# Performance work log

Hardware: AMD Instinct MI355X
Metric: run time of the kernel (lower is better)

Reference implementation:

```python
import jax, jax.numpy as jnp
import numpy as np

N, F_NODE, F_EDGE = 1024, 64, 32
F_IN = 2 * F_NODE + F_EDGE  # 160


def setup_inputs() -> dict:
    key = jax.random.key(0)
    ks = jax.random.split(key, 6)
    H = jax.random.normal(ks[0], (N, F_NODE), dtype=jnp.float32)
    A = jax.random.randint(ks[1], (N, N), 0, 2).astype(jnp.float32)
    E = jax.random.normal(ks[2], (N, N, F_EDGE), dtype=jnp.float32)
    # params: reset_parameters_uniform -> U(-s, s), s = 1/sqrt(dim0)
    s = 1.0 / np.sqrt(F_IN)
    W = jax.random.uniform(ks[3], (F_IN, F_NODE), jnp.float32, -s, s)
    W_att = jax.random.uniform(ks[4], (F_IN, F_NODE), jnp.float32, -s, s)
    sb = 1.0 / np.sqrt(F_NODE)
    bias = jax.random.uniform(ks[5], (F_NODE,), jnp.float32, -sb, sb)
    return {"H": H, "A": A, "E": E, "W": W, "W_att": W_att, "bias": bias}


def reference(H, A, E, W, W_att, bias):
    n = H.shape[0]
    # all-pairs concat: HE[a,b] = [H[a], H[b], E[a,b]]  -> [N, N, 2F+Fe]
    H_row = jnp.broadcast_to(H[:, None, :], (n, n, H.shape[1]))  # H2: repeat over dim 1
    H_col = jnp.broadcast_to(H[None, :, :], (n, n, H.shape[1]))  # H1: repeat over dim 0
    HE = jnp.concatenate([H_row, H_col, E], axis=2) * A[:, :, None]
    Hp = jnp.einsum('abi,ij->abj', HE, W) + bias
    Ha = jnp.einsum('abi,ij->abj', HE, W_att) + bias
    gated = jax.nn.relu(Hp) * jax.nn.sigmoid(Ha)
    return jnp.sum(gated, axis=1)
```

## Files before the change

### kernel.cpp

```cpp
#include <hip/hip_runtime.h>

#define NN 1024
#define FN 64
#define FE 32
#define FIN 160
#define NS 2

typedef __bf16 bf16x8 __attribute__((ext_vector_type(8)));
typedef short  short8 __attribute__((ext_vector_type(8)));
typedef float  f32x4  __attribute__((ext_vector_type(4)));

static __device__ __forceinline__ unsigned short f2b(float x){
    unsigned int u = __float_as_uint(x);
    unsigned int r = (u + 0x7fffu + ((u >> 16) & 1u)) >> 16;
    return (unsigned short)r;
}

static __device__ __forceinline__ float fast_sigmoid(float y){
    return __builtin_amdgcn_rcpf(1.0f + __expf(-y));
}

static __device__ __forceinline__ bf16x8 ldfrag(const unsigned short* p){
    return __builtin_bit_cast(bf16x8, *(const short8*)(p));
}

static __device__ __forceinline__ unsigned packtrunc(float lo, float hi){
    return __builtin_amdgcn_perm(__float_as_uint(hi), __float_as_uint(lo), 0x07060302u);
}

__global__ void prep(const float* __restrict__ H, const float* __restrict__ W,
                     const float* __restrict__ Wa,
                     unsigned short* __restrict__ Hb,
                     unsigned short* __restrict__ WtE,
                     unsigned short* __restrict__ WtA){
    int bid = blockIdx.x, tid = threadIdx.x;
    if (bid < 64){
        int i = (bid*256 + tid)*4;
        float4 v = *(const float4*)(H + i);
        ushort4 o;
        o.x = f2b(v.x); o.y = f2b(v.y); o.z = f2b(v.z); o.w = f2b(v.w);
        *(ushort4*)(Hb + i) = o;
    } else {
        const float* src = (bid == 64) ? W : Wa;
        unsigned short* dst = (bid == 64) ? WtE : WtA;
        for (int idx = tid; idx < FIN*FN; idx += 256){
            int k = idx >> 6, j = idx & 63;
            dst[j*FIN + k] = f2b(src[idx]);
        }
    }
}

__global__ void compact(const float* __restrict__ A, unsigned short* __restrict__ idxg,
                        int* __restrict__ cnt){
    int a = blockIdx.x, tid = threadIdx.x;
    int wave = tid >> 6, lane = tid & 63;
    int b0 = wave*256 + lane*4;
    float4 v = *(const float4*)(A + (size_t)a*NN + b0);
    unsigned short loc[4]; int m = 0;
    if (v.x != 0.f) loc[m++] = (unsigned short)(b0);
    if (v.y != 0.f) loc[m++] = (unsigned short)(b0 + 1);
    if (v.z != 0.f) loc[m++] = (unsigned short)(b0 + 2);
    if (v.w != 0.f) loc[m++] = (unsigned short)(b0 + 3);
    int sc = m;
    #pragma unroll
    for (int d = 1; d < 64; d <<= 1){
        int t = __shfl_up(sc, d, 64);
        sc += (lane >= d) ? t : 0;
    }
    __shared__ int wsum[4];
    if (lane == 63) wsum[wave] = sc;
    __syncthreads();
    int base = 0;
    #pragma unroll
    for (int w = 0; w < 4; w++) base += (w < wave) ? wsum[w] : 0;
    int pos = base + sc - m;
    for (int i = 0; i < m; i++) idxg[(size_t)a*NN + pos + i] = loc[i];
    if (tid == 0) cnt[a] = wsum[0] + wsum[1] + wsum[2] + wsum[3];
}

__global__ __launch_bounds__(256, 3) void mga_main(
    const float* __restrict__ E,
    const unsigned short* __restrict__ Hb,
    const unsigned short* __restrict__ WtE, const unsigned short* __restrict__ WtA,
    const unsigned short* __restrict__ idxg, const int* __restrict__ cnt,
    const float* __restrict__ bias, float* __restrict__ part)
{
    int bid  = blockIdx.x;
    int a    = bid >> 1, s = bid & 1;
    int tid  = threadIdx.x;
    int wave = tid >> 6, lane = tid & 63;
    int col  = lane & 15, quad = lane >> 4;
    int half = wave >> 1, mh = wave & 1;

    __shared__ unsigned short lidx[512];
    __shared__ float red[16*FN];

    int c1   = cnt[a];
    int hlen = (c1 + 1) >> 1;
    int win  = s ? hlen : 0;
    int len  = s ? (c1 - hlen) : hlen;
    int npad = (len + 63) & ~63;

    for (int i = tid; i < npad; i += 256){
        int off = (i < len) ? i : (len - 1);
        lidx[i] = idxg[(size_t)a*NN + win + off];
    }

    bf16x8 Bw[2][3], Ba[2][3];
    #pragma unroll
    for (int tl = 0; tl < 2; tl++){
        int n = (2*half + tl)*16 + col;
        #pragma unroll
        for (int sg = 0; sg < 3; sg++){
            Bw[tl][sg] = ldfrag(WtE + n*FIN + (sg+2)*32 + quad*8);
            Ba[tl][sg] = ldfrag(WtA + n*FIN + (sg+2)*32 + quad*8);
        }
    }

    bf16x8 ha0 = ldfrag(Hb + a*FN + quad*8);
    bf16x8 ha1 = ldfrag(Hb + a*FN + 32 + quad*8);
    f32x4 cw[2], ca[2];
    float acc[2] = {0.f, 0.f};
    #pragma unroll
    for (int tl = 0; tl < 2; tl++){
        int n = (2*half + tl)*16 + col;
        float bj = bias[n];
        f32x4 cb = {bj, bj, bj, bj};
        bf16x8 b0 = ldfrag(WtE + n*FIN + quad*8);
        bf16x8 b1 = ldfrag(WtE + n*FIN + 32 + quad*8);
        cw[tl] = __builtin_amdgcn_mfma_f32_16x16x32_bf16(ha1, b1,
                 __builtin_amdgcn_mfma_f32_16x16x32_bf16(ha0, b0, cb, 0,0,0), 0,0,0);
        b0 = ldfrag(WtA + n*FIN + quad*8);
        b1 = ldfrag(WtA + n*FIN + 32 + quad*8);
        ca[tl] = __builtin_amdgcn_mfma_f32_16x16x32_bf16(ha1, b1,
                 __builtin_amdgcn_mfma_f32_16x16x32_bf16(ha0, b0, cb, 0,0,0), 0,0,0);
    }

    __syncthreads();

    float4 e0[2][2], e1[2][2]; bf16x8 h0[2][2], h1[2][2];

    auto loadsub = [&](int p, int sub){
        #pragma unroll
        for (int mt = 0; mt < 2; mt++){
            int r = lidx[p + mh*32 + mt*16 + col] & (NN - 1);
            const float* ep = E + ((size_t)a*NN + r)*FE + quad*8;
            e0[sub][mt] = *(const float4*)(ep);
            e1[sub][mt] = *(const float4*)(ep + 4);
            h0[sub][mt] = ldfrag(Hb + r*FN + quad*8);
            h1[sub][mt] = ldfrag(Hb + r*FN + 32 + quad*8);
        }
    };

    auto compsub = [&](int p, int sub){
        bool full = (p + 64) <= len;
        #pragma unroll
        for (int mt = 0; mt < 2; mt++){
            int4 pk;
            pk.x = (int)packtrunc(e0[sub][mt].x, e0[sub][mt].y);
            pk.y = (int)packtrunc(e0[sub][mt].z, e0[sub][mt].w);
            pk.z = (int)packtrunc(e1[sub][mt].x, e1[sub][mt].y);
            pk.w = (int)packtrunc(e1[sub][mt].z, e1[sub][mt].w);
            bf16x8 ef = __builtin_bit_cast(bf16x8, pk);
            #pragma unroll
            for (int tl = 0; tl < 2; tl++){
                f32x4 pw = __builtin_amdgcn_mfma_f32_16x16x32_bf16(ef, Bw[tl][2],
                           __builtin_amdgcn_mfma_f32_16x16x32_bf16(h1[sub][mt], Bw[tl][1],
                           __builtin_amdgcn_mfma_f32_16x16x32_bf16(h0[sub][mt], Bw[tl][0],
                               cw[tl], 0,0,0), 0,0,0), 0,0,0);
                f32x4 pa = __builtin_amdgcn_mfma_f32_16x16x32_bf16(ef, Ba[tl][2],
                           __builtin_amdgcn_mfma_f32_16x16x32_bf16(h1[sub][mt], Ba[tl][1],
                           __builtin_amdgcn_mfma_f32_16x16x32_bf16(h0[sub][mt], Ba[tl][0],
                               ca[tl], 0,0,0), 0,0,0), 0,0,0);
                if (full){
                    #pragma unroll
                    for (int r = 0; r < 4; r++)
                        acc[tl] += fmaxf(pw[r], 0.f) * fast_sigmoid(pa[r]);
                } else {
                    #pragma unroll
                    for (int r = 0; r < 4; r++){
                        int pos = p + mh*32 + mt*16 + quad*4 + r;
                        float f = fmaxf(pw[r], 0.f) * fast_sigmoid(pa[r]);
                        acc[tl] += (pos < len) ? f : 0.f;
                    }
                }
            }
        }
    };

    for (int p = 0; p < npad; p += 128){
        bool hasB = (p + 64) < npad;
        loadsub(p, 0);
        if (hasB) loadsub(p + 64, 1);
        compsub(p, 0);
        if (hasB) compsub(p + 64, 1);
    }

    #pragma unroll
    for (int tl = 0; tl < 2; tl++)
        red[(wave*4 + quad)*FN + (2*half + tl)*16 + col] = acc[tl];
    __syncthreads();
    if (tid < FN){
        int base = (tid >= 32) ? 8 : 0;
        float sum = 0.f;
        #pragma unroll
        for (int r = 0; r < 8; r++) sum += red[(base + r)*FN + tid];
        part[((size_t)s*NN + a)*FN + tid] = sum;
    }
}

__global__ void mga_reduce(const float* __restrict__ part, const int* __restrict__ cnt,
                           const float* __restrict__ bias, float* __restrict__ out){
    int i = blockIdx.x*256 + threadIdx.x;
    int a = i >> 6, j = i & 63;
    float bj = bias[j];
    float g0 = fmaxf(bj, 0.f) * fast_sigmoid(bj);
    float c0 = (float)(NN - cnt[a]);
    out[i] = part[i] + part[(size_t)NN*FN + i] + c0 * g0;
}

extern "C" void kernel_launch(void* const* d_in, const int* in_sizes, int n_in,
                              void* d_out, int out_size, void* d_ws, size_t ws_size,
                              hipStream_t stream) {
    const float* H    = (const float*)d_in[0];
    const float* A    = (const float*)d_in[1];
    const float* E    = (const float*)d_in[2];
    const float* W    = (const float*)d_in[3];
    const float* Wa   = (const float*)d_in[4];
    const float* bias = (const float*)d_in[5];
    float* out = (float*)d_out;

    unsigned short* Hb   = (unsigned short*)d_ws;
    unsigned short* WtE  = Hb + NN*FN;
    unsigned short* WtA  = WtE + FN*FIN;
    unsigned short* idxg = WtA + FN*FIN;
    int*            cnt  = (int*)(idxg + (size_t)NN*NN);
    float*          part = (float*)(cnt + NN);

    prep      <<<dim3(66),    dim3(256), 0, stream>>>(H, W, Wa, Hb, WtE, WtA);
    compact   <<<dim3(NN),    dim3(256), 0, stream>>>(A, idxg, cnt);
    mga_main  <<<dim3(NN*NS), dim3(256), 0, stream>>>(E, Hb, WtE, WtA, idxg, cnt, bias, part);
    mga_reduce<<<dim3(256),   dim3(256), 0, stream>>>(part, cnt, bias, out);
}
```

Measured before the change: 240.2 us.

## Fuse adjacency compaction and final reduction into one per-row main kernel

Moves the per-row nonzero compaction of A into the main kernel's shared memory and writes the final output, including the bias term for masked pairs, directly from each block. This removes the compact and reduce kernel launches and the global index/partial round-trips. In exchange, each row now runs on one block instead of two, which halves the grid to 1024 blocks and doubles per-block work.

```diff
diff --git a/kernel.cpp b/kernel.cpp
--- a/kernel.cpp
+++ b/kernel.cpp
@@ -4,7 +4,6 @@
 #define FN 64
 #define FE 32
 #define FIN 160
-#define NS 2
 
 typedef __bf16 bf16x8 __attribute__((ext_vector_type(8)));
 typedef short  short8 __attribute__((ext_vector_type(8)));
@@ -50,61 +49,25 @@
     }
 }
 
-__global__ void compact(const float* __restrict__ A, unsigned short* __restrict__ idxg,
-                        int* __restrict__ cnt){
-    int a = blockIdx.x, tid = threadIdx.x;
-    int wave = tid >> 6, lane = tid & 63;
-    int b0 = wave*256 + lane*4;
-    float4 v = *(const float4*)(A + (size_t)a*NN + b0);
-    unsigned short loc[4]; int m = 0;
-    if (v.x != 0.f) loc[m++] = (unsigned short)(b0);
-    if (v.y != 0.f) loc[m++] = (unsigned short)(b0 + 1);
-    if (v.z != 0.f) loc[m++] = (unsigned short)(b0 + 2);
-    if (v.w != 0.f) loc[m++] = (unsigned short)(b0 + 3);
-    int sc = m;
-    #pragma unroll
-    for (int d = 1; d < 64; d <<= 1){
-        int t = __shfl_up(sc, d, 64);
-        sc += (lane >= d) ? t : 0;
-    }
-    __shared__ int wsum[4];
-    if (lane == 63) wsum[wave] = sc;
-    __syncthreads();
-    int base = 0;
-    #pragma unroll
-    for (int w = 0; w < 4; w++) base += (w < wave) ? wsum[w] : 0;
-    int pos = base + sc - m;
-    for (int i = 0; i < m; i++) idxg[(size_t)a*NN + pos + i] = loc[i];
-    if (tid == 0) cnt[a] = wsum[0] + wsum[1] + wsum[2] + wsum[3];
-}
-
-__global__ __launch_bounds__(256, 3) void mga_main(
+__global__ __launch_bounds__(256, 3) void mga_fused(
+    const float* __restrict__ A,
     const float* __restrict__ E,
     const unsigned short* __restrict__ Hb,
     const unsigned short* __restrict__ WtE, const unsigned short* __restrict__ WtA,
-    const unsigned short* __restrict__ idxg, const int* __restrict__ cnt,
-    const float* __restrict__ bias, float* __restrict__ part)
+    const float* __restrict__ bias, float* __restrict__ out)
 {
-    int bid  = blockIdx.x;
-    int a    = bid >> 1, s = bid & 1;
+    int a    = blockIdx.x;
     int tid  = threadIdx.x;
     int wave = tid >> 6, lane = tid & 63;
     int col  = lane & 15, quad = lane >> 4;
     int half = wave >> 1, mh = wave & 1;
 
-    __shared__ unsigned short lidx[512];
+    __shared__ unsigned short lidx[NN];
     __shared__ float red[16*FN];
-
-    int c1   = cnt[a];
-    int hlen = (c1 + 1) >> 1;
-    int win  = s ? hlen : 0;
-    int len  = s ? (c1 - hlen) : hlen;
-    int npad = (len + 63) & ~63;
-
-    for (int i = tid; i < npad; i += 256){
-        int off = (i < len) ? i : (len - 1);
-        lidx[i] = idxg[(size_t)a*NN + win + off];
-    }
+    __shared__ int wsum[4];
+
+    int b0 = wave*256 + lane*4;
+    float4 av = *(const float4*)(A + (size_t)a*NN + b0);
 
     bf16x8 Bw[2][3], Ba[2][3];
     #pragma unroll
@@ -126,16 +89,47 @@
         int n = (2*half + tl)*16 + col;
         float bj = bias[n];
         f32x4 cb = {bj, bj, bj, bj};
-        bf16x8 b0 = ldfrag(WtE + n*FIN + quad*8);
-        bf16x8 b1 = ldfrag(WtE + n*FIN + 32 + quad*8);
-        cw[tl] = __builtin_amdgcn_mfma_f32_16x16x32_bf16(ha1, b1,
-                 __builtin_amdgcn_mfma_f32_16x16x32_bf16(ha0, b0, cb, 0,0,0), 0,0,0);
-        b0 = ldfrag(WtA + n*FIN + quad*8);
-        b1 = ldfrag(WtA + n*FIN + 32 + quad*8);
-        ca[tl] = __builtin_amdgcn_mfma_f32_16x16x32_bf16(ha1, b1,
-                 __builtin_amdgcn_mfma_f32_16x16x32_bf16(ha0, b0, cb, 0,0,0), 0,0,0);
-    }
-
+        bf16x8 w0 = ldfrag(WtE + n*FIN + quad*8);
+        bf16x8 w1 = ldfrag(WtE + n*FIN + 32 + quad*8);
+        cw[tl] = __builtin_amdgcn_mfma_f32_16x16x32_bf16(ha1, w1,
+                 __builtin_amdgcn_mfma_f32_16x16x32_bf16(ha0, w0, cb, 0,0,0), 0,0,0);
+        w0 = ldfrag(WtA + n*FIN + quad*8);
+        w1 = ldfrag(WtA + n*FIN + 32 + quad*8);
+        ca[tl] = __builtin_amdgcn_mfma_f32_16x16x32_bf16(ha1, w1,
+                 __builtin_amdgcn_mfma_f32_16x16x32_bf16(ha0, w0, cb, 0,0,0), 0,0,0);
+    }
+
+    int m = 0;
+    m += (av.x != 0.f) ? 1 : 0;
+    m += (av.y != 0.f) ? 1 : 0;
+    m += (av.z != 0.f) ? 1 : 0;
+    m += (av.w != 0.f) ? 1 : 0;
+    int sc = m;
+    #pragma unroll
+    for (int d = 1; d < 64; d <<= 1){
+        int t = __shfl_up(sc, d, 64);
+        sc += (lane >= d) ? t : 0;
+    }
+    if (lane == 63) wsum[wave] = sc;
+    __syncthreads();
+    int base = 0;
+    #pragma unroll
+    for (int w = 0; w < 4; w++) base += (w < wave) ? wsum[w] : 0;
+    int c1 = wsum[0] + wsum[1] + wsum[2] + wsum[3];
+    int pos = base + sc - m;
+    {
+        int pp = pos;
+        if (av.x != 0.f) lidx[pp++] = (unsigned short)(b0);
+        if (av.y != 0.f) lidx[pp++] = (unsigned short)(b0 + 1);
+        if (av.z != 0.f) lidx[pp++] = (unsigned short)(b0 + 2);
+        if (av.w != 0.f) lidx[pp++] = (unsigned short)(b0 + 3);
+    }
+    __syncthreads();
+    int npad = (c1 + 63) & ~63;
+    if (c1 > 0){
+        unsigned short last = lidx[c1 - 1];
+        for (int i = c1 + tid; i < npad; i += 256) lidx[i] = last;
+    }
     __syncthreads();
 
     float4 e0[2][2], e1[2][2]; bf16x8 h0[2][2], h1[2][2];
@@ -153,7 +147,7 @@
     };
 
     auto compsub = [&](int p, int sub){
-        bool full = (p + 64) <= len;
+        bool full = (p + 64) <= c1;
         #pragma unroll
         for (int mt = 0; mt < 2; mt++){
             int4 pk;
@@ -179,9 +173,9 @@
                 } else {
                     #pragma unroll
                     for (int r = 0; r < 4; r++){
-                        int pos = p + mh*32 + mt*16 + quad*4 + r;
+                        int ps = p + mh*32 + mt*16 + quad*4 + r;
                         float f = fmaxf(pw[r], 0.f) * fast_sigmoid(pa[r]);
-                        acc[tl] += (pos < len) ? f : 0.f;
+                        acc[tl] += (ps < c1) ? f : 0.f;
                     }
                 }
             }
@@ -201,22 +195,14 @@
         red[(wave*4 + quad)*FN + (2*half + tl)*16 + col] = acc[tl];
     __syncthreads();
     if (tid < FN){
-        int base = (tid >= 32) ? 8 : 0;
+        int rbase = (tid >= 32) ? 8 : 0;
         float sum = 0.f;
         #pragma unroll
-        for (int r = 0; r < 8; r++) sum += red[(base + r)*FN + tid];
-        part[((size_t)s*NN + a)*FN + tid] = sum;
-    }
-}
-
-__global__ void mga_reduce(const float* __restrict__ part, const int* __restrict__ cnt,
-                           const float* __restrict__ bias, float* __restrict__ out){
-    int i = blockIdx.x*256 + threadIdx.x;
-    int a = i >> 6, j = i & 63;
-    float bj = bias[j];
-    float g0 = fmaxf(bj, 0.f) * fast_sigmoid(bj);
-    float c0 = (float)(NN - cnt[a]);
-    out[i] = part[i] + part[(size_t)NN*FN + i] + c0 * g0;
+        for (int r = 0; r < 8; r++) sum += red[(rbase + r)*FN + tid];
+        float bj = bias[tid];
+        float g0 = fmaxf(bj, 0.f) * fast_sigmoid(bj);
+        out[(size_t)a*FN + tid] = sum + (float)(NN - c1) * g0;
+    }
 }
 
 extern "C" void kernel_launch(void* const* d_in, const int* in_sizes, int n_in,
@@ -233,12 +219,7 @@
     unsigned short* Hb   = (unsigned short*)d_ws;
     unsigned short* WtE  = Hb + NN*FN;
     unsigned short* WtA  = WtE + FN*FIN;
-    unsigned short* idxg = WtA + FN*FIN;
-    int*            cnt  = (int*)(idxg + (size_t)NN*NN);
-    float*          part = (float*)(cnt + NN);
-
-    prep      <<<dim3(66),    dim3(256), 0, stream>>>(H, W, Wa, Hb, WtE, WtA);
-    compact   <<<dim3(NN),    dim3(256), 0, stream>>>(A, idxg, cnt);
-    mga_main  <<<dim3(NN*NS), dim3(256), 0, stream>>>(E, Hb, WtE, WtA, idxg, cnt, bias, part);
-    mga_reduce<<<dim3(256),   dim3(256), 0, stream>>>(part, cnt, bias, out);
-}
+
+    prep     <<<dim3(66), dim3(256), 0, stream>>>(H, W, Wa, Hb, WtE, WtA);
+    mga_fused<<<dim3(NN), dim3(256), 0, stream>>>(A, E, Hb, WtE, WtA, bias, out);
+}
```

After: 229.8 us. -4.3%, faster.
